# Performance work log

Measured on AMD Instinct MI355X. Metric: run time of the kernel, lower is better.

Reference implementation:

```python
import jax, jax.numpy as jnp
import numpy as np

KERNEL_SIZE = 5

def setup_inputs() -> dict:
    key = jax.random.key(0)
    k1, k2, k3 = jax.random.split(key, 3)
    H = W = 4096
    stdv = 1.0 / KERNEL_SIZE
    return {
        "input": jax.random.normal(k1, (H, W), dtype=jnp.float32),
        "K_hit": jax.random.uniform(k2, (KERNEL_SIZE, KERNEL_SIZE), dtype=jnp.float32, minval=-stdv, maxval=stdv),
        "K_miss": jax.random.uniform(k3, (KERNEL_SIZE, KERNEL_SIZE), dtype=jnp.float32, minval=-stdv, maxval=stdv),
    }

def _hitmiss(x, K_hit, K_miss):
    k = K_hit.shape[0]
    c = (k - 1) // 2
    Hout = x.shape[0] - 2 * c
    Wout = x.shape[1] - 2 * c
    # Fmap[i,j] = min_{di,dj}(x[i+di, j+dj] - K_hit[di,dj]) - max_{di,dj}(x[i+di, j+dj] - K_miss[di,dj])
    mn = jnp.full((Hout, Wout), jnp.inf, dtype=x.dtype)
    mx = jnp.full((Hout, Wout), -jnp.inf, dtype=x.dtype)
    for di in range(k):          # small fixed k*k loop over structuring-element offsets
        for dj in range(k):
            w = x[di:di + Hout, dj:dj + Wout]
            mn = jnp.minimum(mn, w - K_hit[di, dj])
            mx = jnp.maximum(mx, w - K_miss[di, dj])
    return mn - mx

def reference(input, K_hit, K_miss):
    return _hitmiss(input, K_hit, K_miss)
```

## Files before the change

kernel.cpp:

```cpp
#include <hip/hip_runtime.h>
#include <math.h>


constexpr int KS = 5;
constexpr int WW = 4096;
constexpr int HO = 4092;
constexpr int WO = 4092;
constexpr int CG = WO / 4;
constexpr int RPT = 2;

__device__ __forceinline__ float min3f(float a, float b, float c) {
    float d;
    asm("v_min3_f32 %0, %1, %2, %3" : "=v"(d) : "v"(a), "v"(b), "v"(c));
    return d;
}
__device__ __forceinline__ float max3f(float a, float b, float c) {
    float d;
    asm("v_max3_f32 %0, %1, %2, %3" : "=v"(d) : "v"(a), "v"(b), "v"(c));
    return d;
}

__global__ __launch_bounds__(256) void hitmiss_kernel(
    const float* __restrict__ x,
    const float* __restrict__ kh,
    const float* __restrict__ km,
    float* __restrict__ out)
{
    const int cg = blockIdx.x * blockDim.x + threadIdx.x;
    if (cg >= CG) return;
    const int j0 = cg * 4;
    const int r0 = blockIdx.y * RPT;

    float wh[KS * KS], wm[KS * KS];
#pragma unroll
    for (int i = 0; i < KS * KS; ++i) {
        wh[i] = kh[i];
        wm[i] = km[i];
    }

    float v[RPT + 4][8];
#pragma unroll
    for (int r = 0; r < RPT + 4; ++r) {
        const float* rp = x + (size_t)(r0 + r) * WW + j0;
        float4 a = *reinterpret_cast<const float4*>(rp);
        float4 b = *reinterpret_cast<const float4*>(rp + 4);
        v[r][0] = a.x; v[r][1] = a.y; v[r][2] = a.z; v[r][3] = a.w;
        v[r][4] = b.x; v[r][5] = b.y; v[r][6] = b.z; v[r][7] = b.w;
    }

#pragma unroll
    for (int orow = 0; orow < RPT; ++orow) {
        float mnA[4], mxA[4], mnP[4], mxP[4];

#pragma unroll
        for (int di = 0; di < KS; ++di) {
#pragma unroll
            for (int dj = 0; dj < KS; ++dj) {
                const int k = di * KS + dj;
                const float h = wh[k];
                const float m = wm[k];
#pragma unroll
                for (int p = 0; p < 4; ++p) {
                    const float t  = v[orow + di][dj + p];
                    const float th = t - h;
                    const float tm = t - m;
                    if (k == 0) {
                        mnA[p] = th; mxA[p] = tm;
                    } else if (k & 1) {
                        mnP[p] = th; mxP[p] = tm;
                    } else {
                        mnA[p] = min3f(mnA[p], mnP[p], th);
                        mxA[p] = max3f(mxA[p], mxP[p], tm);
                    }
                }
            }
        }

        float4 o;
        o.x = mnA[0] - mxA[0];
        o.y = mnA[1] - mxA[1];
        o.z = mnA[2] - mxA[2];
        o.w = mnA[3] - mxA[3];
        *reinterpret_cast<float4*>(out + (size_t)(r0 + orow) * WO + j0) = o;
    }
}

extern "C" void kernel_launch(void* const* d_in, const int* in_sizes, int n_in,
                              void* d_out, int out_size, void* d_ws, size_t ws_size,
                              hipStream_t stream) {
    const float* x  = (const float*)d_in[0];
    const float* kh = (const float*)d_in[1];
    const float* km = (const float*)d_in[2];
    float* out = (float*)d_out;

    dim3 block(256, 1, 1);
    dim3 grid((CG + 255) / 256, HO / RPT, 1);
    hipLaunchKernelGGL(hitmiss_kernel, grid, block, 0, stream, x, kh, km, out);
}
```

Before: 126.2 us.

## Stage input tiles in LDS and compute 8 rows per thread

Replaces per-thread direct global float4 loads of overlapping row windows with a cooperative load of a 260x36 input tile into shared memory. Each thread then reads its 5-row stencil windows from LDS and produces 8 output rows of 4 columns. This is meant to cut the redundant global/L2 traffic from halo overlap between threads and rows. The cost is a block-wide barrier, about 37KB of LDS per block, and edge clamping with guarded stores.

```diff
diff --git a/kernel.cpp b/kernel.cpp
--- a/kernel.cpp
+++ b/kernel.cpp
@@ -4,10 +4,16 @@
 
 constexpr int KS = 5;
 constexpr int WW = 4096;
+constexpr int HH = 4096;
 constexpr int HO = 4092;
 constexpr int WO = 4092;
-constexpr int CG = WO / 4;
-constexpr int RPT = 2;
+
+constexpr int TW  = 256;
+constexpr int TH  = 32;
+constexpr int IW  = TW + KS - 1;
+constexpr int IH  = TH + KS - 1;
+constexpr int F4W = IW / 4;
+constexpr int NF4 = F4W * IH;
 
 __device__ __forceinline__ float min3f(float a, float b, float c) {
     float d;
@@ -26,10 +32,11 @@
     const float* __restrict__ km,
     float* __restrict__ out)
 {
-    const int cg = blockIdx.x * blockDim.x + threadIdx.x;
-    if (cg >= CG) return;
-    const int j0 = cg * 4;
-    const int r0 = blockIdx.y * RPT;
+    __shared__ __attribute__((aligned(16))) float lds[IW * IH];
+
+    const int tid = threadIdx.x;
+    const int c0  = blockIdx.x * TW;
+    const int r0  = blockIdx.y * TH;
 
     float wh[KS * KS], wm[KS * KS];
 #pragma unroll
@@ -38,22 +45,38 @@
         wm[i] = km[i];
     }
 
-    float v[RPT + 4][8];
 #pragma unroll
-    for (int r = 0; r < RPT + 4; ++r) {
-        const float* rp = x + (size_t)(r0 + r) * WW + j0;
-        float4 a = *reinterpret_cast<const float4*>(rp);
-        float4 b = *reinterpret_cast<const float4*>(rp + 4);
-        v[r][0] = a.x; v[r][1] = a.y; v[r][2] = a.z; v[r][3] = a.w;
-        v[r][4] = b.x; v[r][5] = b.y; v[r][6] = b.z; v[r][7] = b.w;
+    for (int it = 0; it < (NF4 + 255) / 256; ++it) {
+        const int f = it * 256 + tid;
+        if (f < NF4) {
+            const int fr = f / F4W;
+            const int fc = (f - fr * F4W) * 4;
+            int gr = r0 + fr; if (gr > HH - 1) gr = HH - 1;
+            int gc = c0 + fc; if (gc > WW - 4) gc = WW - 4;
+            const float4 a = *reinterpret_cast<const float4*>(x + (size_t)gr * WW + gc);
+            *reinterpret_cast<float4*>(&lds[fr * IW + fc]) = a;
+        }
     }
+    __syncthreads();
+
+    const int tx = tid & 63;
+    const int ty = tid >> 6;
+    const int jl = tx * 4;
+    const int jg = c0 + jl;
+    const bool colok = (jg + 3 < WO);
 
 #pragma unroll
-    for (int orow = 0; orow < RPT; ++orow) {
+    for (int orow = 0; orow < TH / 4; ++orow) {
+        const int s0 = ty * (TH / 4) + orow;
+
         float mnA[4], mxA[4], mnP[4], mxP[4];
 
 #pragma unroll
         for (int di = 0; di < KS; ++di) {
+            const float* lp = &lds[(s0 + di) * IW + jl];
+            const float4 a = *reinterpret_cast<const float4*>(lp);
+            const float4 b = *reinterpret_cast<const float4*>(lp + 4);
+            const float v[8] = {a.x, a.y, a.z, a.w, b.x, b.y, b.z, b.w};
 #pragma unroll
             for (int dj = 0; dj < KS; ++dj) {
                 const int k = di * KS + dj;
@@ -61,7 +84,7 @@
                 const float m = wm[k];
 #pragma unroll
                 for (int p = 0; p < 4; ++p) {
-                    const float t  = v[orow + di][dj + p];
+                    const float t  = v[dj + p];
                     const float th = t - h;
                     const float tm = t - m;
                     if (k == 0) {
@@ -76,12 +99,15 @@
             }
         }
 
-        float4 o;
-        o.x = mnA[0] - mxA[0];
-        o.y = mnA[1] - mxA[1];
-        o.z = mnA[2] - mxA[2];
-        o.w = mnA[3] - mxA[3];
-        *reinterpret_cast<float4*>(out + (size_t)(r0 + orow) * WO + j0) = o;
+        const int og = r0 + s0;
+        if (colok && og < HO) {
+            float4 o;
+            o.x = mnA[0] - mxA[0];
+            o.y = mnA[1] - mxA[1];
+            o.z = mnA[2] - mxA[2];
+            o.w = mnA[3] - mxA[3];
+            *reinterpret_cast<float4*>(out + (size_t)og * WO + jg) = o;
+        }
     }
 }
 
@@ -94,6 +120,6 @@
     float* out = (float*)d_out;
 
     dim3 block(256, 1, 1);
-    dim3 grid((CG + 255) / 256, HO / RPT, 1);
+    dim3 grid((WO + TW - 1) / TW, (HO + TH - 1) / TH, 1);
     hipLaunchKernelGGL(hitmiss_kernel, grid, block, 0, stream, x, kh, km, out);
 }
```

After: 133.7 us. +6.0%, slower.

## Stage per-wave input tiles in LDS via direct global-to-LDS loads

Applied to the files above, without the earlier changes.

Each wave now copies an 8-row by 260-column input strip straight into LDS with global_load_lds. It then computes 4 output rows per thread from that strip, where before each thread loaded its own 6 overlapping rows from global memory to produce 2 output rows. The aim is less redundant global/L2 traffic and more reuse of each input row. The cost is LDS capacity, which is requested as 4 blocks per CU in the launch bounds, plus bounds checks on edge tiles. Correctness depends on the compiler inserting the wait for the asynchronous LDS writes before they are read.

```diff
diff --git a/kernel.cpp b/kernel.cpp
--- a/kernel.cpp
+++ b/kernel.cpp
@@ -4,10 +4,14 @@
 
 constexpr int KS = 5;
 constexpr int WW = 4096;
+constexpr int HH = 4096;
 constexpr int HO = 4092;
 constexpr int WO = 4092;
-constexpr int CG = WO / 4;
-constexpr int RPT = 2;
+
+constexpr int WROWS = 4;
+constexpr int IROWS = WROWS + KS - 1;
+constexpr int IWF   = 260;
+constexpr int WLDS  = IROWS * IWF;
 
 __device__ __forceinline__ float min3f(float a, float b, float c) {
     float d;
@@ -20,16 +24,24 @@
     return d;
 }
 
-__global__ __launch_bounds__(256) void hitmiss_kernel(
+typedef __attribute__((address_space(1))) const void gvoid;
+typedef __attribute__((address_space(3))) void svoid;
+
+__global__ __launch_bounds__(256, 4) void hitmiss_kernel(
     const float* __restrict__ x,
     const float* __restrict__ kh,
     const float* __restrict__ km,
     float* __restrict__ out)
 {
-    const int cg = blockIdx.x * blockDim.x + threadIdx.x;
-    if (cg >= CG) return;
-    const int j0 = cg * 4;
-    const int r0 = blockIdx.y * RPT;
+    __shared__ __attribute__((aligned(16))) float lds[4 * WLDS];
+
+    const int tid  = threadIdx.x;
+    const int w    = tid >> 6;
+    const int lane = tid & 63;
+    const int c0   = blockIdx.x * 256;
+    const int r0w  = blockIdx.y * 16 + w * 4;
+
+    float* ldsw = &lds[w * WLDS];
 
     float wh[KS * KS], wm[KS * KS];
 #pragma unroll
@@ -38,22 +50,35 @@
         wm[i] = km[i];
     }
 
-    float v[RPT + 4][8];
+    {
+        const int gc1 = c0 + lane * 4;
+        int gc2 = c0 + 256; if (gc2 > WW - 4) gc2 = WW - 4;
 #pragma unroll
-    for (int r = 0; r < RPT + 4; ++r) {
-        const float* rp = x + (size_t)(r0 + r) * WW + j0;
-        float4 a = *reinterpret_cast<const float4*>(rp);
-        float4 b = *reinterpret_cast<const float4*>(rp + 4);
-        v[r][0] = a.x; v[r][1] = a.y; v[r][2] = a.z; v[r][3] = a.w;
-        v[r][4] = b.x; v[r][5] = b.y; v[r][6] = b.z; v[r][7] = b.w;
+        for (int r = 0; r < IROWS; ++r) {
+            int gr = r0w + r; if (gr > HH - 1) gr = HH - 1;
+            const float* gp1 = x + (size_t)gr * WW + gc1;
+            __builtin_amdgcn_global_load_lds((gvoid*)gp1, (svoid*)(ldsw + r * IWF), 16, 0, 0);
+            if (lane < 1) {
+                const float* gp2 = x + (size_t)gr * WW + gc2;
+                __builtin_amdgcn_global_load_lds((gvoid*)gp2, (svoid*)(ldsw + r * IWF + 256), 16, 0, 0);
+            }
+        }
     }
 
+    const int jl = lane * 4;
+    const int jg = c0 + jl;
+    const bool colok = (jg <= WO - 4);
+
 #pragma unroll
-    for (int orow = 0; orow < RPT; ++orow) {
+    for (int orow = 0; orow < WROWS; ++orow) {
         float mnA[4], mxA[4], mnP[4], mxP[4];
 
 #pragma unroll
         for (int di = 0; di < KS; ++di) {
+            const float* lp = ldsw + (orow + di) * IWF + jl;
+            const float4 a = *reinterpret_cast<const float4*>(lp);
+            const float4 b = *reinterpret_cast<const float4*>(lp + 4);
+            const float v[8] = {a.x, a.y, a.z, a.w, b.x, b.y, b.z, b.w};
 #pragma unroll
             for (int dj = 0; dj < KS; ++dj) {
                 const int k = di * KS + dj;
@@ -61,7 +86,7 @@
                 const float m = wm[k];
 #pragma unroll
                 for (int p = 0; p < 4; ++p) {
-                    const float t  = v[orow + di][dj + p];
+                    const float t  = v[dj + p];
                     const float th = t - h;
                     const float tm = t - m;
                     if (k == 0) {
@@ -76,12 +101,15 @@
             }
         }
 
-        float4 o;
-        o.x = mnA[0] - mxA[0];
-        o.y = mnA[1] - mxA[1];
-        o.z = mnA[2] - mxA[2];
-        o.w = mnA[3] - mxA[3];
-        *reinterpret_cast<float4*>(out + (size_t)(r0 + orow) * WO + j0) = o;
+        const int og = r0w + orow;
+        if (colok && og < HO) {
+            float4 o;
+            o.x = mnA[0] - mxA[0];
+            o.y = mnA[1] - mxA[1];
+            o.z = mnA[2] - mxA[2];
+            o.w = mnA[3] - mxA[3];
+            *reinterpret_cast<float4*>(out + (size_t)og * WO + jg) = o;
+        }
     }
 }
 
@@ -94,6 +122,6 @@
     float* out = (float*)d_out;
 
     dim3 block(256, 1, 1);
-    dim3 grid((CG + 255) / 256, HO / RPT, 1);
+    dim3 grid((WO + 255) / 256, (HO + 15) / 16, 1);
     hipLaunchKernelGGL(hitmiss_kernel, grid, block, 0, stream, x, kh, km, out);
 }
```

Result: no change. 128.2 us (+1.6%).

## Stream rows through a rolling five-row register window per wavefront

Applied to the files above, without the earlier changes.

Each wavefront now covers 256 columns and 10 consecutive output rows. It keeps a rotating window of five input rows in registers and loads only one new row per output row, instead of reloading six rows for every two outputs. The goal is to cut redundant global/L2 input traffic and the per-thread load overhead. Filter weights are now read directly from uniform memory at each use. The trade-off is more register pressure, with launch bounds set to 4 blocks, and clamped edge loads plus guarded stores for the ragged tail.

```diff
diff --git a/kernel.cpp b/kernel.cpp
--- a/kernel.cpp
+++ b/kernel.cpp
@@ -2,12 +2,12 @@
 #include <math.h>
 
 
-constexpr int KS = 5;
-constexpr int WW = 4096;
-constexpr int HO = 4092;
-constexpr int WO = 4092;
-constexpr int CG = WO / 4;
-constexpr int RPT = 2;
+constexpr int KS  = 5;
+constexpr int WW  = 4096;
+constexpr int HH  = 4096;
+constexpr int HO  = 4092;
+constexpr int WO  = 4092;
+constexpr int RPT = 10;
 
 __device__ __forceinline__ float min3f(float a, float b, float c) {
     float d;
@@ -20,69 +20,94 @@
     return d;
 }
 
-__global__ __launch_bounds__(256) void hitmiss_kernel(
+template<int DI>
+__device__ __forceinline__ void rowupd(float4 A, float4 B,
+    const float* __restrict__ kh, const float* __restrict__ km,
+    float (&mnA)[4], float (&mxA)[4], float (&mnP)[4], float (&mxP)[4])
+{
+    const float v[8] = {A.x, A.y, A.z, A.w, B.x, B.y, B.z, B.w};
+#pragma unroll
+    for (int dj = 0; dj < KS; ++dj) {
+        const int k = DI * KS + dj;
+        const float h = kh[k];
+        const float m = km[k];
+#pragma unroll
+        for (int p = 0; p < 4; ++p) {
+            const float t  = v[dj + p];
+            const float th = t - h;
+            const float tm = t - m;
+            if (k == 0) {
+                mnA[p] = th; mxA[p] = tm;
+            } else if (k & 1) {
+                mnP[p] = th; mxP[p] = tm;
+            } else {
+                mnA[p] = min3f(mnA[p], mnP[p], th);
+                mxA[p] = max3f(mxA[p], mxP[p], tm);
+            }
+        }
+    }
+}
+
+#define LOADROW(A, B, T) do {                                              \
+    int gr_ = r0w + (T); if (gr_ > HH - 1) gr_ = HH - 1;                   \
+    const float* rp_ = x + (size_t)gr_ * WW;                               \
+    (A) = *reinterpret_cast<const float4*>(rp_ + gc1);                     \
+    (B) = *reinterpret_cast<const float4*>(rp_ + gc2);                     \
+} while (0)
+
+#define STEP(A0,B0,A1,B1,A2,B2,A3,B3,A4,B4, T, DOLOAD) do {                \
+    float mnA[4], mxA[4], mnP[4], mxP[4];                                  \
+    rowupd<0>(A0, B0, kh, km, mnA, mxA, mnP, mxP);                         \
+    rowupd<1>(A1, B1, kh, km, mnA, mxA, mnP, mxP);                         \
+    rowupd<2>(A2, B2, kh, km, mnA, mxA, mnP, mxP);                         \
+    rowupd<3>(A3, B3, kh, km, mnA, mxA, mnP, mxP);                         \
+    rowupd<4>(A4, B4, kh, km, mnA, mxA, mnP, mxP);                         \
+    const int og_ = r0w + (T);                                             \
+    if (colok && og_ < HO) {                                               \
+        float4 o_;                                                         \
+        o_.x = mnA[0] - mxA[0];                                            \
+        o_.y = mnA[1] - mxA[1];                                            \
+        o_.z = mnA[2] - mxA[2];                                            \
+        o_.w = mnA[3] - mxA[3];                                            \
+        *reinterpret_cast<float4*>(out + (size_t)og_ * WO + jg) = o_;      \
+    }                                                                      \
+    if (DOLOAD) LOADROW(A0, B0, (T) + 5);                                  \
+} while (0)
+
+__global__ __launch_bounds__(256, 4) void hitmiss_kernel(
     const float* __restrict__ x,
     const float* __restrict__ kh,
     const float* __restrict__ km,
     float* __restrict__ out)
 {
-    const int cg = blockIdx.x * blockDim.x + threadIdx.x;
-    if (cg >= CG) return;
-    const int j0 = cg * 4;
-    const int r0 = blockIdx.y * RPT;
+    const int tid  = threadIdx.x;
+    const int w    = tid >> 6;
+    const int lane = tid & 63;
+    const int c0   = blockIdx.x * 256;
+    const int r0w  = (blockIdx.y * 4 + w) * RPT;
 
-    float wh[KS * KS], wm[KS * KS];
-#pragma unroll
-    for (int i = 0; i < KS * KS; ++i) {
-        wh[i] = kh[i];
-        wm[i] = km[i];
-    }
+    const int gc1 = c0 + lane * 4;
+    int gc2 = gc1 + 4; if (gc2 > WW - 4) gc2 = WW - 4;
+    const int jg = gc1;
+    const bool colok = (jg <= WO - 4);
 
-    float v[RPT + 4][8];
-#pragma unroll
-    for (int r = 0; r < RPT + 4; ++r) {
-        const float* rp = x + (size_t)(r0 + r) * WW + j0;
-        float4 a = *reinterpret_cast<const float4*>(rp);
-        float4 b = *reinterpret_cast<const float4*>(rp + 4);
-        v[r][0] = a.x; v[r][1] = a.y; v[r][2] = a.z; v[r][3] = a.w;
-        v[r][4] = b.x; v[r][5] = b.y; v[r][6] = b.z; v[r][7] = b.w;
-    }
+    float4 a0, b0, a1, b1, a2, b2, a3, b3, a4, b4;
+    LOADROW(a0, b0, 0);
+    LOADROW(a1, b1, 1);
+    LOADROW(a2, b2, 2);
+    LOADROW(a3, b3, 3);
+    LOADROW(a4, b4, 4);
 
-#pragma unroll
-    for (int orow = 0; orow < RPT; ++orow) {
-        float mnA[4], mxA[4], mnP[4], mxP[4];
-
-#pragma unroll
-        for (int di = 0; di < KS; ++di) {
-#pragma unroll
-            for (int dj = 0; dj < KS; ++dj) {
-                const int k = di * KS + dj;
-                const float h = wh[k];
-                const float m = wm[k];
-#pragma unroll
-                for (int p = 0; p < 4; ++p) {
-                    const float t  = v[orow + di][dj + p];
-                    const float th = t - h;
-                    const float tm = t - m;
-                    if (k == 0) {
-                        mnA[p] = th; mxA[p] = tm;
-                    } else if (k & 1) {
-                        mnP[p] = th; mxP[p] = tm;
-                    } else {
-                        mnA[p] = min3f(mnA[p], mnP[p], th);
-                        mxA[p] = max3f(mxA[p], mxP[p], tm);
-                    }
-                }
-            }
-        }
-
-        float4 o;
-        o.x = mnA[0] - mxA[0];
-        o.y = mnA[1] - mxA[1];
-        o.z = mnA[2] - mxA[2];
-        o.w = mnA[3] - mxA[3];
-        *reinterpret_cast<float4*>(out + (size_t)(r0 + orow) * WO + j0) = o;
-    }
+    STEP(a0,b0, a1,b1, a2,b2, a3,b3, a4,b4, 0, true);
+    STEP(a1,b1, a2,b2, a3,b3, a4,b4, a0,b0, 1, true);
+    STEP(a2,b2, a3,b3, a4,b4, a0,b0, a1,b1, 2, true);
+    STEP(a3,b3, a4,b4, a0,b0, a1,b1, a2,b2, 3, true);
+    STEP(a4,b4, a0,b0, a1,b1, a2,b2, a3,b3, 4, true);
+    STEP(a0,b0, a1,b1, a2,b2, a3,b3, a4,b4, 5, true);
+    STEP(a1,b1, a2,b2, a3,b3, a4,b4, a0,b0, 6, true);
+    STEP(a2,b2, a3,b3, a4,b4, a0,b0, a1,b1, 7, true);
+    STEP(a3,b3, a4,b4, a0,b0, a1,b1, a2,b2, 8, true);
+    STEP(a4,b4, a0,b0, a1,b1, a2,b2, a3,b3, 9, false);
 }
 
 extern "C" void kernel_launch(void* const* d_in, const int* in_sizes, int n_in,
@@ -94,6 +119,6 @@
     float* out = (float*)d_out;
 
     dim3 block(256, 1, 1);
-    dim3 grid((CG + 255) / 256, HO / RPT, 1);
+    dim3 grid((WO + 255) / 256, (HO + 4 * RPT - 1) / (4 * RPT), 1);
     hipLaunchKernelGGL(hitmiss_kernel, grid, block, 0, stream, x, kh, km, out);
 }
```

Result: no change. 127.2 us (+0.9%).
